# Optimization experiments

Measured on AMD Instinct MI355X. Metric: run time of the kernel, lower is better.

Reference implementation:

```python
import jax, jax.numpy as jnp
import numpy as np
from jax import lax

# Static config (matches init_kwargs / electrode montage)
B, T, V = 16, 1536, 64
F1, D, H = 16, 2, 4
F2 = F1 * D              # 32
FO = F2 // H             # 8, GAT per-head out dim
K1, K3 = 32, 16          # conv kernel sizes (temporal)
P1, P2 = 8, 4            # avg pool sizes
KNN = 4
EPS = 1e-5
NEG_SLOPE = 0.2          # PyG GATConv leaky_relu slope


def _build_edges():
    # deterministic electrode geometry -> kNN graph, plus PyG self-loops
    rng = np.random.RandomState(0)
    pos = rng.randn(V, 3)
    dmat = np.linalg.norm(pos[:, None] - pos[None, :], axis=-1)
    order = np.argsort(dmat, axis=1)
    nbrs = order[:, 1:KNN + 1]                      # exclude self
    src = np.repeat(np.arange(V), KNN)
    dst = nbrs.reshape(-1)
    # add self loops (GATConv default add_self_loops=True)
    src = np.concatenate([src, np.arange(V)])
    dst = np.concatenate([dst, np.arange(V)])
    return jnp.asarray(np.stack([src, dst]), dtype=jnp.int32)  # (2, E)


def _bn(x, g, b, m, v, axis):
    shp = [1] * x.ndim
    shp[axis] = -1
    rs = lambda a: a.reshape(shp)
    return rs(g) * (x - rs(m)) * lax.rsqrt(rs(v) + EPS) + rs(b)


def _conv_same_t(x, w, k):
    # Conv2d(..., (1,k), padding='same'): torch pads (k-1)//2 left, rest right
    lp = (k - 1) // 2
    return lax.conv_general_dilated(x, w, (1, 1), [(0, 0), (lp, k - 1 - lp)],
                                    dimension_numbers=('NCHW', 'OIHW', 'NCHW'))


def _gat(x, W, a_src, a_dst, bias, src, dst):
    # Batched PyG GATConv (eval mode, dropout off), concat heads.
    # x: (Ng, V, F1); W: (F1, H*FO); a_src/a_dst: (H, FO); bias: (H*FO,)
    Ng = x.shape[0]
    h = jnp.einsum('nvf,fho->nvho', x, W.reshape(F1, H, FO))   # (Ng,V,H,FO)
    es = jnp.einsum('nvho,ho->nvh', h, a_src)[:, src]          # (Ng,E,H)
    ed = jnp.einsum('nvho,ho->nvh', h, a_dst)[:, dst]
    e = jax.nn.leaky_relu(es + ed, NEG_SLOPE)
    # softmax over incoming edges of each target node (segment softmax)
    m = jnp.full((Ng, V, H), -1e30, e.dtype).at[:, dst].max(e)
    ex = jnp.exp(e - m[:, dst])
    den = jnp.zeros((Ng, V, H), e.dtype).at[:, dst].add(ex)
    alpha = ex / den[:, dst]                                   # (Ng,E,H)
    out = jnp.zeros((Ng, V, H, FO), e.dtype).at[:, dst].add(alpha[..., None] * h[:, src])
    return out.reshape(Ng, V, H * FO) + bias


def setup_inputs() -> dict:
    key = jax.random.key(0)
    ks = jax.random.split(key, 16)
    bn = lambda k, c: (1.0 + 0.1 * jax.random.normal(jax.random.fold_in(k, 0), (c,)),
                       0.1 * jax.random.normal(jax.random.fold_in(k, 1), (c,)),
                       0.1 * jax.random.normal(jax.random.fold_in(k, 2), (c,)),
                       0.5 + jax.random.uniform(jax.random.fold_in(k, 3), (c,)))
    bn1 = bn(ks[1], F1); bn2 = bn(ks[2], F2); bn3 = bn(ks[3], F2)
    inp = {
        'x': jax.random.normal(ks[0], (B, 1, V, T), jnp.float32),
        'conv1_w': 0.1 * jax.random.normal(ks[4], (F1, 1, 1, K1), jnp.float32),
        'bn1_g': bn1[0], 'bn1_b': bn1[1], 'bn1_m': bn1[2], 'bn1_v': bn1[3],
        'gat_w': (1.0 / np.sqrt(F1)) * jax.random.normal(ks[5], (F1, H * FO), jnp.float32),
        'gat_asrc': 0.3 * jax.random.normal(ks[6], (H, FO), jnp.float32),
        'gat_adst': 0.3 * jax.random.normal(ks[7], (H, FO), jnp.float32),
        'gat_bias': 0.05 * jax.random.normal(ks[8], (H * FO,), jnp.float32),
        'bn2_g': bn2[0], 'bn2_b': bn2[1], 'bn2_m': bn2[2], 'bn2_v': bn2[3],
        'conv3_w': 0.1 * jax.random.normal(ks[9], (F2, F2, 1, K3), jnp.float32),
        'bn3_g': bn3[0], 'bn3_b': bn3[1], 'bn3_m': bn3[2], 'bn3_v': bn3[3],
        'edge_index': _build_edges(),
    }
    return inp


def reference(x, conv1_w, bn1_g, bn1_b, bn1_m, bn1_v,
              gat_w, gat_asrc, gat_adst, gat_bias,
              bn2_g, bn2_b, bn2_m, bn2_v,
              conv3_w, bn3_g, bn3_b, bn3_m, bn3_v, edge_index):
    src, dst = edge_index[0], edge_index[1]
    # block1: temporal conv + BN
    h = _conv_same_t(x, conv1_w, K1)                 # (B,F1,V,T)
    h = _bn(h, bn1_g, bn1_b, bn1_m, bn1_v, 1)
    # spatial GNN over B*T independent electrode graphs
    xg = h.transpose(0, 3, 2, 1).reshape(B * T, V, F1)
    g = _gat(xg, gat_w, gat_asrc, gat_adst, gat_bias, src, dst)   # (BT,V,F2)
    g = g.mean(axis=1).reshape(B, T, F2).transpose(0, 2, 1)       # (B,F2,T)
    g = _bn(g, bn2_g, bn2_b, bn2_m, bn2_v, 1)[:, :, None, :]      # (B,F2,1,T)
    # tail: elu -> pool -> conv -> bn -> elu -> pool (dropout = eval no-op)
    h = jax.nn.elu(g)
    h = h.reshape(B, F2, 1, T // P1, P1).mean(-1)
    h = _conv_same_t(h, conv3_w, K3)
    h = _bn(h, bn3_g, bn3_b, bn3_m, bn3_v, 1)
    h = jax.nn.elu(h)
    h = h.reshape(B, F2, 1, T // P1 // P2, P2).mean(-1)           # (B,F2,1,48)
    return h
```

## Files before the change

### kernel.cpp

```cpp
#include <hip/hip_runtime.h>
#include <math.h>

#define TPB 256

constexpr int Bc = 16, Tc = 1536;
constexpr int T2c = 192;
constexpr float EPSc = 1e-5f;
constexpr float NSLOPE = 0.2f;
constexpr int MDI = 16;
constexpr int MDO = 8;
constexpr float L2E = 1.4426950408889634f;

constexpr int TILE = 16;
constexpr int ROWS = 48;

typedef float vf2 __attribute__((ext_vector_type(2)));

constexpr int OW_WEFF = 0;
constexpr int OW_CHL  = 1024;
constexpr int OW_CES  = 1056;
constexpr int OW_WSD  = 1064;
constexpr int OW_A2C2 = 1320;
constexpr int OW_WFT  = 1384;
constexpr int OW_GRAPH= 2408;
constexpr int OW_P    = 2825;

constexpr int L_XT  = 0;
constexpr int L_WB  = 3264;
constexpr int L_TOT = 7616;

#define LGKM0() __asm__ volatile("s_waitcnt lgkmcnt(0)" ::: "memory")

__device__ __forceinline__ int xt_idx(int row, int g, int lo)
{
    return L_XT + row * 68 + (((g + row) & 15) << 2) + lo;
}

__device__ __forceinline__ float lexp2(float z)
{
    return __builtin_amdgcn_exp2f(fmaxf(z, NSLOPE * z));
}

__device__ __forceinline__ float bfly16_sum(float s)
{
#if __has_builtin(__builtin_amdgcn_permlane16_swap)
    unsigned u = __builtin_bit_cast(unsigned, s);
    auto r = __builtin_amdgcn_permlane16_swap(u, u, false, false);
    return __builtin_bit_cast(float, (unsigned)r[0]) +
           __builtin_bit_cast(float, (unsigned)r[1]);
#else
    return s + __shfl_xor(s, 16);
#endif
}

__device__ __forceinline__ float bfly32_sum(float s)
{
#if __has_builtin(__builtin_amdgcn_permlane32_swap)
    unsigned u = __builtin_bit_cast(unsigned, s);
    auto r = __builtin_amdgcn_permlane32_swap(u, u, false, false);
    return __builtin_bit_cast(float, (unsigned)r[0]) +
           __builtin_bit_cast(float, (unsigned)r[1]);
#else
    return s + __shfl_xor(s, 32);
#endif
}

__global__ void prep_kernel(const float* __restrict__ c1w,
                            const float* __restrict__ g1, const float* __restrict__ b1,
                            const float* __restrict__ m1, const float* __restrict__ v1,
                            const float* __restrict__ W,
                            const float* __restrict__ asrc, const float* __restrict__ adst,
                            const float* __restrict__ bias,
                            const float* __restrict__ g2, const float* __restrict__ b2,
                            const float* __restrict__ m2, const float* __restrict__ v2,
                            const int* __restrict__ ei, int ne, float* __restrict__ ws)
{
    const int tid = threadIdx.x;
    __shared__ float sweff[1024];
    __shared__ float schl[32];
    __shared__ int isrcp_i[64 * MDI];
    __shared__ int outdst_i[64 * MDO];
    __shared__ int inslot[64], outslot[64];

    for (int idx = tid; idx < 1024; idx += TPB) {
        int k = idx >> 5, f2 = idx & 31;
        float s = 0.f;
        for (int f = 0; f < 16; f++) {
            float a1 = g1[f] * rsqrtf(v1[f] + EPSc);
            s += a1 * W[f * 32 + f2] * c1w[f * 32 + k];
        }
        ws[OW_WEFF + idx] = s;
        ws[OW_WFT + f2 * 32 + k] = s;
        sweff[idx] = s;
    }
    for (int f2 = tid; f2 < 32; f2 += TPB) {
        float s = 0.f;
        for (int f = 0; f < 16; f++) {
            float a1 = g1[f] * rsqrtf(v1[f] + EPSc);
            s = fmaf(b1[f] - a1 * m1[f], W[f * 32 + f2], s);
        }
        ws[OW_CHL + f2] = s;
        schl[f2] = s;
        float a2 = g2[f2] * rsqrtf(v2[f2] + EPSc);
        ws[OW_A2C2 + f2] = a2;
        ws[OW_A2C2 + 32 + f2] = b2[f2] + a2 * (bias[f2] - m2[f2] + s);
    }

    for (int i = tid; i < 64 * MDI; i += TPB) isrcp_i[i] = 0;
    for (int i = tid; i < 64 * MDO; i += TPB) outdst_i[i] = 0;
    if (tid < 64) { inslot[tid] = 0; outslot[tid] = 0; }
    __syncthreads();
    for (int e = tid; e < ne; e += TPB) {
        int s = ei[e], d = ei[ne + e];
        if (s == d) continue;
        int pi = atomicAdd(&inslot[d], 1);
        if (pi < 15) isrcp_i[d * MDI + pi] = s;
        int po = atomicAdd(&outslot[s], 1);
        if (po < MDO) outdst_i[s * MDO + po] = d;
    }
    __syncthreads();

    if (tid < 128) {
        int k = tid >> 2, h = tid & 3;
        float s1 = 0.f, s2 = 0.f;
        for (int o = 0; o < 8; o++) {
            float wv = sweff[k * 32 + h * 8 + o];
            s1 = fmaf(asrc[h * 8 + o], wv, s1);
            s2 = fmaf(adst[h * 8 + o], wv, s2);
        }
        ws[OW_WSD + h * 64 + k * 2]     = s1;
        ws[OW_WSD + h * 64 + k * 2 + 1] = s2;
    }
    if (tid < 4) {
        float s1 = 0.f, s2 = 0.f;
        for (int o = 0; o < 8; o++) {
            float cv = schl[tid * 8 + o];
            s1 = fmaf(asrc[tid * 8 + o], cv, s1);
            s2 = fmaf(adst[tid * 8 + o], cv, s2);
        }
        ws[OW_CES + tid * 2]     = s1;
        ws[OW_CES + tid * 2 + 1] = s2;
    }
    unsigned char* gb = (unsigned char*)(ws + OW_GRAPH);
    for (int i = tid; i < 64 * MDI; i += TPB) gb[i] = (unsigned char)isrcp_i[i];
    for (int i = tid; i < 64 * MDO; i += TPB) gb[1088 + i] = (unsigned char)outdst_i[i];
    __syncthreads();
    if (tid < 64) {
        int id = inslot[tid] < 15 ? inslot[tid] : 15;
        int od = outslot[tid] < MDO ? outslot[tid] : MDO;
        gb[tid * MDI + 15] = (unsigned char)id;
        gb[1024 + tid] = (unsigned char)id;
        gb[1600 + tid] = (unsigned char)od;
    }
    __syncthreads();
    if (tid == 0) {
        int mi = 0;
        for (int d = 0; d < 64; d++) {
            int a = gb[1024 + d];
            mi = a > mi ? a : mi;
        }
        gb[1664] = (unsigned char)mi;
        gb[1665] = 0;
    }
}

__global__ __launch_bounds__(TPB, 4) void gat_kernel(
    const float* __restrict__ x,
    const float* __restrict__ wfTp,
    const float* __restrict__ cesg,
    const float* __restrict__ wsdg,
    const float* __restrict__ a2c2,
    const int* __restrict__ graphi,
    float* __restrict__ pout)
{
    __shared__ __align__(16) float sm[L_TOT];

    const int tid   = threadIdx.x;
    const int b     = blockIdx.x / 96;
    const int tile2 = blockIdx.x % 96;
    const int t0    = tile2 * TILE;

    const int h = tid >> 6, v = tid & 63;

    const unsigned char* gbg = (const unsigned char*)graphi;
    const int4 il = *(const int4*)(gbg + v * MDI);
    const unsigned ow = *(const unsigned*)(gbg + 1088 + v * MDO);
    const int mdin = __builtin_amdgcn_readfirstlane(((const int*)graphi)[416] & 0xFF);

    for (int idx = tid; idx < ROWS * 64; idx += TPB) {
        const int vv = idx / ROWS, j = idx % ROWS;
        float val = 1.0f;
        if (j < 47) {
            const int t = t0 - 15 + j;
            val = (t >= 0 && t < Tc) ? x[(b * 64 + vv) * Tc + t] : 0.f;
        }
        sm[xt_idx(j, vv >> 2, vv & 3)] = val;
    }
    __syncthreads();

    const int hs = __builtin_amdgcn_readfirstlane(h);
    const vf2* wsdh = (const vf2*)(wsdg + hs * 64);

    float aes[16], aed[16];
    {
        const int g = v >> 2, lo = v & 3;
        const vf2 cv = *(const vf2*)(cesg + hs * 2);
        vf2 acc2[16];
        #pragma unroll
        for (int t = 0; t < 16; t++) acc2[t] = cv;
        float xr[16];
        #pragma unroll
        for (int q = 0; q < 15; q++) xr[q] = sm[xt_idx(q, g, lo)];
        #pragma unroll
        for (int k = 0; k < 32; k++) {
            xr[(k + 15) & 15] = sm[xt_idx(k + 15, g, lo)];
            const vf2 wk = wsdh[k];
            #pragma unroll
            for (int t = 0; t < 16; t++) {
                const float xv = xr[(k + t) & 15];
                acc2[t] += (vf2){xv, xv} * wk;
            }
        }
        #pragma unroll
        for (int t = 0; t < 16; t++) {
            aes[t] = acc2[t].x * L2E;
            aed[t] = acc2[t].y * L2E;
        }
    }

    {
        float* scr0 = &sm[L_WB + h * 1088];
        float* scr1 = &sm[L_WB + h * 1088 + 272];
        float* scr2 = &sm[L_WB + h * 1088 + 544];
        float* scr3 = &sm[L_WB + h * 1088 + 816];

        const int indeg = (int)(((unsigned)il.w) >> 24);
        const unsigned iw[4] = {(unsigned)il.x, (unsigned)il.y,
                                (unsigned)il.z, (unsigned)il.w};

        float den[16], Eself[16];
        #pragma unroll
        for (int t = 0; t < 16; t++) {
            Eself[t] = lexp2(aes[t] + aed[t]);
            den[t] = Eself[t];
        }

        *(float4*)(scr0 + v * 4) = (float4){aes[0],  aes[1],  aes[2],  aes[3]};
        *(float4*)(scr1 + v * 4) = (float4){aes[4],  aes[5],  aes[6],  aes[7]};
        *(float4*)(scr2 + v * 4) = (float4){aes[8],  aes[9],  aes[10], aes[11]};
        *(float4*)(scr3 + v * 4) = (float4){aes[12], aes[13], aes[14], aes[15]};
        LGKM0();
        #pragma unroll
        for (int e = 0; e < 15; e++) {
            if (e < mdin) {
                const int s = (int)((iw[e >> 2] >> ((e & 3) * 8)) & 0xFF);
                const float4 ea = *(const float4*)(scr0 + s * 4);
                const float4 eb = *(const float4*)(scr1 + s * 4);
                const float4 ec = *(const float4*)(scr2 + s * 4);
                const float4 ed = *(const float4*)(scr3 + s * 4);
                const float valid = (e < indeg) ? 1.f : 0.f;
                den[0]  += valid * lexp2(ea.x + aed[0]);
                den[1]  += valid * lexp2(ea.y + aed[1]);
                den[2]  += valid * lexp2(ea.z + aed[2]);
                den[3]  += valid * lexp2(ea.w + aed[3]);
                den[4]  += valid * lexp2(eb.x + aed[4]);
                den[5]  += valid * lexp2(eb.y + aed[5]);
                den[6]  += valid * lexp2(eb.z + aed[6]);
                den[7]  += valid * lexp2(eb.w + aed[7]);
                den[8]  += valid * lexp2(ec.x + aed[8]);
                den[9]  += valid * lexp2(ec.y + aed[9]);
                den[10] += valid * lexp2(ec.z + aed[10]);
                den[11] += valid * lexp2(ec.w + aed[11]);
                den[12] += valid * lexp2(ed.x + aed[12]);
                den[13] += valid * lexp2(ed.y + aed[13]);
                den[14] += valid * lexp2(ed.z + aed[14]);
                den[15] += valid * lexp2(ed.w + aed[15]);
            }
        }
        LGKM0();

        float rden[16], wb[16];
        #pragma unroll
        for (int t = 0; t < 16; t++) {
            float r = __builtin_amdgcn_rcpf(den[t]);
            r = r * (2.f - den[t] * r);
            rden[t] = r;
            wb[t] = Eself[t] * r;
        }

        #pragma unroll
        for (int r2 = 0; r2 < 2; r2++) {
            const int tb = r2 * 8;
            *(float4*)(scr0 + v * 4) = (float4){aed[tb + 0], aed[tb + 1],
                                                rden[tb + 0], rden[tb + 1]};
            *(float4*)(scr1 + v * 4) = (float4){aed[tb + 2], aed[tb + 3],
                                                rden[tb + 2], rden[tb + 3]};
            *(float4*)(scr2 + v * 4) = (float4){aed[tb + 4], aed[tb + 5],
                                                rden[tb + 4], rden[tb + 5]};
            *(float4*)(scr3 + v * 4) = (float4){aed[tb + 6], aed[tb + 7],
                                                rden[tb + 6], rden[tb + 7]};
            LGKM0();
            #pragma unroll
            for (int j = 0; j < 4; j++) {
                const int d = (int)((ow >> (j * 8)) & 0xFF);
                const float4 g0 = *(const float4*)(scr0 + d * 4);
                const float4 g1 = *(const float4*)(scr1 + d * 4);
                const float4 g2 = *(const float4*)(scr2 + d * 4);
                const float4 g3 = *(const float4*)(scr3 + d * 4);
                wb[tb + 0] = fmaf(lexp2(aes[tb + 0] + g0.x), g0.z, wb[tb + 0]);
                wb[tb + 1] = fmaf(lexp2(aes[tb + 1] + g0.y), g0.w, wb[tb + 1]);
                wb[tb + 2] = fmaf(lexp2(aes[tb + 2] + g1.x), g1.z, wb[tb + 2]);
                wb[tb + 3] = fmaf(lexp2(aes[tb + 3] + g1.y), g1.w, wb[tb + 3]);
                wb[tb + 4] = fmaf(lexp2(aes[tb + 4] + g2.x), g2.z, wb[tb + 4]);
                wb[tb + 5] = fmaf(lexp2(aes[tb + 5] + g2.y), g2.w, wb[tb + 5]);
                wb[tb + 6] = fmaf(lexp2(aes[tb + 6] + g3.x), g3.z, wb[tb + 6]);
                wb[tb + 7] = fmaf(lexp2(aes[tb + 7] + g3.y), g3.w, wb[tb + 7]);
            }
            LGKM0();
        }

        #pragma unroll
        for (int t = 0; t < 16; t++)
            sm[L_WB + h * 1088 + t * 68 + v] = wb[t];
    }
    LGKM0();

    {
        const int cg = v & 7;
        const int th = (v >> 3) & 1;
        const int kq = v >> 4;

        #pragma unroll
        for (int rep = 0; rep < 2; rep++) {
            vf2 yp[4][6];
            #pragma unroll
            for (int i = 0; i < 4; i++)
                #pragma unroll
                for (int q = 0; q < 6; q++) yp[i][q] = (vf2){0.f, 0.f};

            const float* wbbase = &sm[L_WB + h * 1088 + (rep * 8 + th * 4) * 68];
            #pragma unroll
            for (int v4 = 0; v4 < 4; v4++) {
                const int vcol = kq * 16 + v4 * 4;
                float4 wrow[4];
                #pragma unroll
                for (int i = 0; i < 4; i++)
                    wrow[i] = *(const float4*)(wbbase + i * 68 + vcol);
                #pragma unroll
                for (int q = 0; q < 6; q++) {
                    const int row = cg * 6 + q;
                    const int mg = ((kq * 4 + v4 + row) & 15) << 2;
                    const float4 x4 = *(const float4*)(&sm[L_XT + row * 68 + mg]);
                    const vf2 x01 = (vf2){x4.x, x4.y}, x23 = (vf2){x4.z, x4.w};
                    #pragma unroll
                    for (int i = 0; i < 4; i++) {
                        const vf2 w01 = (vf2){wrow[i].x, wrow[i].y};
                        const vf2 w23 = (vf2){wrow[i].z, wrow[i].w};
                        yp[i][q] += w01 * x01;
                        yp[i][q] += w23 * x23;
                    }
                }
            }
            float ya[4][6];
            #pragma unroll
            for (int i = 0; i < 4; i++)
                #pragma unroll
                for (int q = 0; q < 6; q++) {
                    float s = yp[i][q].x + yp[i][q].y;
                    ya[i][q] = bfly32_sum(bfly16_sum(s));
                }
            float* yw = &sm[L_WB + h * 1088 + (rep * 8 + th * 4 + kq) * 49 + cg * 6];
            #pragma unroll
            for (int q = 0; q < 6; q++) {
                float a01 = (kq & 1) ? ya[1][q] : ya[0][q];
                float a23 = (kq & 1) ? ya[3][q] : ya[2][q];
                yw[q] = (kq & 2) ? a23 : a01;
            }
        }
    }
    LGKM0();

    {
        const int t = v >> 3, o = v & 7;
        const int f2d = h * 8 + o;
        const float4* wf4 = (const float4*)(wfTp + f2d * 32);
        const float a2 = a2c2[f2d], c2 = a2c2[32 + f2d];

        #pragma unroll
        for (int po = 0; po < 2; po++) {
            const int tt = po * 8 + t;
            const float* yr = &sm[L_WB + h * 1088 + tt * 49];
            float acc = 0.f;
            #pragma unroll
            for (int k4 = 0; k4 < 8; k4++) {
                const float4 w = wf4[k4];
                acc = fmaf(w.x, yr[tt + 4 * k4 + 0],
                      fmaf(w.y, yr[tt + 4 * k4 + 1],
                      fmaf(w.z, yr[tt + 4 * k4 + 2],
                      fmaf(w.w, yr[tt + 4 * k4 + 3], acc))));
            }
            float y = fmaf(a2, acc * (1.f / 64.f), c2);
            y = y > 0.f ? y : __expf(y) - 1.f;
            y += __shfl_xor(y, 8);
            y = bfly32_sum(bfly16_sum(y));
            if (v < 8)
                pout[(b * T2c + tile2 * 2 + po) * 32 + h * 8 + v] = y * 0.125f;
        }
    }
}

__global__ __launch_bounds__(TPB) void conv3_kernel(const float* __restrict__ pp,
                                                    const float* __restrict__ w3,
                                                    const float* __restrict__ g3,
                                                    const float* __restrict__ b3,
                                                    const float* __restrict__ m3,
                                                    const float* __restrict__ v3,
                                                    float* __restrict__ outp)
{
    __shared__ float pl[63 * 32];
    __shared__ float q[48 * 32];
    const int tid = threadIdx.x;
    const int b = blockIdx.x >> 2, cc = blockIdx.x & 3;

    for (int idx = tid; idx < 63 * 32; idx += TPB) {
        int r = idx >> 5, f2 = idx & 31;
        int tog = cc * 48 - 7 + r;
        pl[idx] = (tog >= 0 && tog < T2c) ? pp[(b * T2c + tog) * 32 + f2] : 0.f;
    }
    __syncthreads();

    const int f2o = tid & 31, grp = tid >> 5;
    const int tb = grp * 6;
    float acc[6] = { 0.f, 0.f, 0.f, 0.f, 0.f, 0.f };
    for (int f2i = 0; f2i < 32; f2i++) {
        float seg[21];
        #pragma unroll
        for (int r = 0; r < 21; r++) seg[r] = pl[(tb + r) * 32 + f2i];
        const float4* wrow = (const float4*)(w3 + (f2o * 32 + f2i) * 16);
        #pragma unroll
        for (int k4 = 0; k4 < 4; k4++) {
            const float4 w4 = wrow[k4];
            #pragma unroll
            for (int j = 0; j < 6; j++) {
                acc[j] = fmaf(seg[j + k4 * 4 + 0], w4.x,
                         fmaf(seg[j + k4 * 4 + 1], w4.y,
                         fmaf(seg[j + k4 * 4 + 2], w4.z,
                         fmaf(seg[j + k4 * 4 + 3], w4.w, acc[j]))));
            }
        }
    }
    const float a3 = g3[f2o] * rsqrtf(v3[f2o] + EPSc);
    const float c3 = b3[f2o] - a3 * m3[f2o];
    #pragma unroll
    for (int j = 0; j < 6; j++) {
        float y = fmaf(a3, acc[j], c3);
        y = y > 0.f ? y : __expf(y) - 1.f;
        q[(tb + j) * 32 + f2o] = y;
    }
    __syncthreads();
    for (int idx = tid; idx < 12 * 32; idx += TPB) {
        int t4 = idx >> 5, f2 = idx & 31;
        int r0 = t4 * 4;
        float s = q[r0 * 32 + f2] + q[(r0 + 1) * 32 + f2] +
                  q[(r0 + 2) * 32 + f2] + q[(r0 + 3) * 32 + f2];
        outp[(b * 32 + f2) * 48 + cc * 12 + t4] = s * 0.25f;
    }
}

extern "C" void kernel_launch(void* const* d_in, const int* in_sizes, int n_in,
                              void* d_out, int out_size, void* d_ws, size_t ws_size,
                              hipStream_t stream)
{
    const float* x    = (const float*)d_in[0];
    const float* c1w  = (const float*)d_in[1];
    const float* g1   = (const float*)d_in[2];
    const float* b1   = (const float*)d_in[3];
    const float* m1   = (const float*)d_in[4];
    const float* v1   = (const float*)d_in[5];
    const float* W    = (const float*)d_in[6];
    const float* asrc = (const float*)d_in[7];
    const float* adst = (const float*)d_in[8];
    const float* bias = (const float*)d_in[9];
    const float* g2   = (const float*)d_in[10];
    const float* b2   = (const float*)d_in[11];
    const float* m2   = (const float*)d_in[12];
    const float* v2   = (const float*)d_in[13];
    const float* w3   = (const float*)d_in[14];
    const float* g3   = (const float*)d_in[15];
    const float* b3   = (const float*)d_in[16];
    const float* m3   = (const float*)d_in[17];
    const float* v3   = (const float*)d_in[18];
    const int*   ei   = (const int*)d_in[19];
    const int    ne   = in_sizes[19] / 2;

    float* ws = (float*)d_ws;

    prep_kernel<<<1, TPB, 0, stream>>>(c1w, g1, b1, m1, v1, W, asrc, adst,
                                       bias, g2, b2, m2, v2, ei, ne, ws);

    gat_kernel<<<Bc * 96, TPB, 0, stream>>>(x,
                                            ws + OW_WFT,
                                            ws + OW_CES,
                                            ws + OW_WSD,
                                            ws + OW_A2C2,
                                            (const int*)(ws + OW_GRAPH),
                                            ws + OW_P);

    conv3_kernel<<<Bc * 4, TPB, 0, stream>>>(ws + OW_P, w3, g3, b3, m3, v3,
                                             (float*)d_out);
}
```

Measured before the change: 161.0 us.

## Split conv3 across more blocks with transposed LDS tile; hoist BN1 scalars in prep

```diff
diff --git a/kernel.cpp b/kernel.cpp
--- a/kernel.cpp
+++ b/kernel.cpp
@@ -78,27 +78,36 @@
     const int tid = threadIdx.x;
     __shared__ float sweff[1024];
     __shared__ float schl[32];
+    __shared__ float a1s[16], b1ms[16];
     __shared__ int isrcp_i[64 * MDI];
     __shared__ int outdst_i[64 * MDO];
     __shared__ int inslot[64], outslot[64];
 
+    if (tid < 16) {
+        float a1 = g1[tid] * rsqrtf(v1[tid] + EPSc);
+        a1s[tid] = a1;
+        b1ms[tid] = b1[tid] - a1 * m1[tid];
+    }
+    for (int i = tid; i < 64 * MDI; i += TPB) isrcp_i[i] = 0;
+    for (int i = tid; i < 64 * MDO; i += TPB) outdst_i[i] = 0;
+    if (tid < 64) { inslot[tid] = 0; outslot[tid] = 0; }
+    __syncthreads();
+
     for (int idx = tid; idx < 1024; idx += TPB) {
         int k = idx >> 5, f2 = idx & 31;
         float s = 0.f;
-        for (int f = 0; f < 16; f++) {
-            float a1 = g1[f] * rsqrtf(v1[f] + EPSc);
-            s += a1 * W[f * 32 + f2] * c1w[f * 32 + k];
-        }
+        #pragma unroll
+        for (int f = 0; f < 16; f++)
+            s = fmaf(a1s[f] * W[f * 32 + f2], c1w[f * 32 + k], s);
         ws[OW_WEFF + idx] = s;
         ws[OW_WFT + f2 * 32 + k] = s;
         sweff[idx] = s;
     }
     for (int f2 = tid; f2 < 32; f2 += TPB) {
         float s = 0.f;
-        for (int f = 0; f < 16; f++) {
-            float a1 = g1[f] * rsqrtf(v1[f] + EPSc);
-            s = fmaf(b1[f] - a1 * m1[f], W[f * 32 + f2], s);
-        }
+        #pragma unroll
+        for (int f = 0; f < 16; f++)
+            s = fmaf(b1ms[f], W[f * 32 + f2], s);
         ws[OW_CHL + f2] = s;
         schl[f2] = s;
         float a2 = g2[f2] * rsqrtf(v2[f2] + EPSc);
@@ -106,10 +115,6 @@
         ws[OW_A2C2 + 32 + f2] = b2[f2] + a2 * (bias[f2] - m2[f2] + s);
     }
 
-    for (int i = tid; i < 64 * MDI; i += TPB) isrcp_i[i] = 0;
-    for (int i = tid; i < 64 * MDO; i += TPB) outdst_i[i] = 0;
-    if (tid < 64) { inslot[tid] = 0; outslot[tid] = 0; }
-    __syncthreads();
     for (int e = tid; e < ne; e += TPB) {
         int s = ei[e], d = ei[ne + e];
         if (s == d) continue;
@@ -409,7 +414,7 @@
     }
 }
 
-__global__ __launch_bounds__(TPB) void conv3_kernel(const float* __restrict__ pp,
+__global__ __launch_bounds__(192) void conv3_kernel(const float* __restrict__ pp,
                                                     const float* __restrict__ w3,
                                                     const float* __restrict__ g3,
                                                     const float* __restrict__ b3,
@@ -417,31 +422,32 @@
                                                     const float* __restrict__ v3,
                                                     float* __restrict__ outp)
 {
-    __shared__ float pl[63 * 32];
-    __shared__ float q[48 * 32];
+    __shared__ __align__(16) float plT[32 * 42];
+    __shared__ float q[24 * 32];
     const int tid = threadIdx.x;
-    const int b = blockIdx.x >> 2, cc = blockIdx.x & 3;
-
-    for (int idx = tid; idx < 63 * 32; idx += TPB) {
+    const int b = blockIdx.x >> 3, cc = blockIdx.x & 7;
+
+    for (int idx = tid; idx < 39 * 32; idx += 192) {
         int r = idx >> 5, f2 = idx & 31;
-        int tog = cc * 48 - 7 + r;
-        pl[idx] = (tog >= 0 && tog < T2c) ? pp[(b * T2c + tog) * 32 + f2] : 0.f;
+        int tog = cc * 24 - 7 + r;
+        plT[f2 * 42 + r] = (tog >= 0 && tog < T2c) ? pp[(b * T2c + tog) * 32 + f2] : 0.f;
     }
     __syncthreads();
 
     const int f2o = tid & 31, grp = tid >> 5;
-    const int tb = grp * 6;
-    float acc[6] = { 0.f, 0.f, 0.f, 0.f, 0.f, 0.f };
+    const int tb = grp * 4;
+    float acc[4] = { 0.f, 0.f, 0.f, 0.f };
     for (int f2i = 0; f2i < 32; f2i++) {
-        float seg[21];
-        #pragma unroll
-        for (int r = 0; r < 21; r++) seg[r] = pl[(tb + r) * 32 + f2i];
+        float seg[19];
+        const float* base = &plT[f2i * 42 + tb];
+        #pragma unroll
+        for (int r = 0; r < 19; r++) seg[r] = base[r];
         const float4* wrow = (const float4*)(w3 + (f2o * 32 + f2i) * 16);
         #pragma unroll
         for (int k4 = 0; k4 < 4; k4++) {
             const float4 w4 = wrow[k4];
             #pragma unroll
-            for (int j = 0; j < 6; j++) {
+            for (int j = 0; j < 4; j++) {
                 acc[j] = fmaf(seg[j + k4 * 4 + 0], w4.x,
                          fmaf(seg[j + k4 * 4 + 1], w4.y,
                          fmaf(seg[j + k4 * 4 + 2], w4.z,
@@ -452,18 +458,18 @@
     const float a3 = g3[f2o] * rsqrtf(v3[f2o] + EPSc);
     const float c3 = b3[f2o] - a3 * m3[f2o];
     #pragma unroll
-    for (int j = 0; j < 6; j++) {
+    for (int j = 0; j < 4; j++) {
         float y = fmaf(a3, acc[j], c3);
         y = y > 0.f ? y : __expf(y) - 1.f;
         q[(tb + j) * 32 + f2o] = y;
     }
     __syncthreads();
-    for (int idx = tid; idx < 12 * 32; idx += TPB) {
-        int t4 = idx >> 5, f2 = idx & 31;
-        int r0 = t4 * 4;
+    {
+        int t4l = tid >> 5, f2 = tid & 31;
+        int r0 = t4l * 4;
         float s = q[r0 * 32 + f2] + q[(r0 + 1) * 32 + f2] +
                   q[(r0 + 2) * 32 + f2] + q[(r0 + 3) * 32 + f2];
-        outp[(b * 32 + f2) * 48 + cc * 12 + t4] = s * 0.25f;
+        outp[(b * 32 + f2) * 48 + cc * 6 + t4l] = s * 0.25f;
     }
 }
 
@@ -506,6 +512,6 @@
                                             (const int*)(ws + OW_GRAPH),
                                             ws + OW_P);
 
-    conv3_kernel<<<Bc * 4, TPB, 0, stream>>>(ws + OW_P, w3, g3, b3, m3, v3,
+    conv3_kernel<<<Bc * 8, 192, 0, stream>>>(ws + OW_P, w3, g3, b3, m3, v3,
                                              (float*)d_out);
 }
```

New measurement: 156.7 us (median of 2 runs). 1.03x faster.
